# Kernel optimization log

Measured on AMD Instinct MI355X. Metric: run time of the kernel, lower is better.

Reference implementation:

```python
import jax, jax.numpy as jnp
import numpy as np

DIM = 192
HEADS = 8
B, H, W = 8, 128, 128

def _dwconv3x3(x, w):
    # x: [B,C,H,W], w: [C,1,3,3] depthwise
    return jax.lax.conv_general_dilated(
        x, w, window_strides=(1, 1), padding=((1, 1), (1, 1)),
        dimension_numbers=('NCHW', 'OIHW', 'NCHW'),
        feature_group_count=x.shape[1])

def _proj(x, pw, dw):
    # 1x1 pointwise (as einsum) followed by 3x3 depthwise
    y = jnp.einsum('bchw,oc->bohw', x, pw)
    return _dwconv3x3(y, dw)

def setup_inputs() -> dict:
    key = jax.random.key(0)
    ks = jax.random.split(key, 9)
    s_pw = 1.0 / np.sqrt(DIM)
    s_dw = 1.0 / 3.0
    return {
        'x_feat': jax.random.normal(ks[0], (B, DIM, H, W), jnp.float32),
        'y_feat': jax.random.normal(ks[1], (B, DIM, H, W), jnp.float32),
        'q_pw': jax.random.normal(ks[2], (DIM, DIM), jnp.float32) * s_pw,
        'q_dw': jax.random.normal(ks[3], (DIM, 1, 3, 3), jnp.float32) * s_dw,
        'k_pw': jax.random.normal(ks[4], (DIM, DIM), jnp.float32) * s_pw,
        'k_dw': jax.random.normal(ks[5], (DIM, 1, 3, 3), jnp.float32) * s_dw,
        'v_pw': jax.random.normal(ks[6], (DIM, DIM), jnp.float32) * s_pw,
        'v_dw': jax.random.normal(ks[7], (DIM, 1, 3, 3), jnp.float32) * s_dw,
        'proj_w': jax.random.normal(ks[8], (DIM, DIM), jnp.float32) * s_pw,
        'temperature': jnp.ones((HEADS, 1, 1), jnp.float32),
    }

def reference(x_feat, y_feat, q_pw, q_dw, k_pw, k_dw, v_pw, v_dw, proj_w, temperature):
    b, c, h, w = x_feat.shape
    ch = c // HEADS  # channels per head
    q = _proj(x_feat, q_pw, q_dw)
    k = _proj(y_feat, k_pw, k_dw)
    v = _proj(y_feat, v_pw, v_dw)
    # b (head c) h w -> b head c (h w)
    to_heads = lambda t: t.reshape(b, HEADS, ch, h * w)
    q, k, v = to_heads(q), to_heads(k), to_heads(v)
    # L2-normalize along token dim (torch F.normalize eps=1e-12)
    q = q / jnp.maximum(jnp.linalg.norm(q, axis=-1, keepdims=True), 1e-12)
    k = k / jnp.maximum(jnp.linalg.norm(k, axis=-1, keepdims=True), 1e-12)
    attn = jnp.einsum('bhcn,bhdn->bhcd', q, k) * temperature  # [b,heads,ch,ch]
    attn = jax.nn.softmax(attn, axis=-1)
    out = jnp.einsum('bhcd,bhdn->bhcn', attn, v)
    out = out.reshape(b, c, h, w)
    out = jnp.einsum('bchw,oc->bohw', out, proj_w)
    return out
```

## Files before the change

### kernel.cpp

```cpp
#include <hip/hip_runtime.h>
#include <hip/hip_bf16.h>

#define BATCH 8
#define CDIM 192
#define HEADS 8
#define CH 24
#define HH 128
#define WW 128
#define NPIX (HH*WW)
#define NELEM (BATCH*CDIM*NPIX)
#define NP4 (NPIX/4)

#define NSLAB 64
#define NJOBS 624

typedef __attribute__((ext_vector_type(8))) short bf16x8;
typedef __attribute__((ext_vector_type(4))) float f32x4;
typedef __attribute__((ext_vector_type(4))) unsigned int u32x4;
typedef unsigned int u32;
typedef const __attribute__((address_space(1))) u32* gas_ptr;
typedef __attribute__((address_space(3))) u32* las_ptr;

#define UNIT 100663296ull
__device__ __align__(256) unsigned char g_pool[6 * UNIT + (16u << 20)];

#define OFF_T0Q  (0 * UNIT)
#define OFF_T0K  (1 * UNIT)
#define OFF_T0V  (2 * UNIT)
#define OFF_Q    (3 * UNIT)
#define OFF_K    (4 * UNIT)
#define OFF_V    (5 * UNIT)
#define OFF_MISC (6 * UNIT)
#define OFF_PART (OFF_MISC)
#define OFF_S    (OFF_MISC + 10223616ull)
#define OFF_M    (OFF_S + 159744ull)
#define OFF_MF   (OFF_M + 1179648ull)

__device__ inline unsigned short bf_rne(float x) {
  unsigned u = __float_as_uint(x);
  unsigned r = (u + 0x7fffu + ((u >> 16) & 1u)) >> 16;
  return (unsigned short)r;
}
__device__ inline void f32_split(float x, unsigned short& h, unsigned short& l) {
  h = bf_rne(x);
  float hf = __uint_as_float(((unsigned)h) << 16);
  l = bf_rne(x - hf);
}

__global__ __launch_bounds__(64) void w_to_frag(const float* __restrict__ W,
                                                unsigned short* __restrict__ F,
                                                int nb) {
  const int b = blockIdx.x / 12, mf = blockIdx.x % 12;
  const int lane = threadIdx.x;
  const int row = mf * 16 + (lane & 15);
  const size_t lo = (size_t)nb * CDIM * CDIM;
#pragma unroll
  for (int ks = 0; ks < 6; ++ks) {
    const int k0 = ks * 32 + (lane >> 4) * 8;
    const float* src = W + ((size_t)b * CDIM + row) * CDIM + k0;
    bf16x8 hv, lv;
#pragma unroll
    for (int j = 0; j < 8; ++j) {
      unsigned short h, l;
      f32_split(src[j], h, l);
      hv[j] = (short)h;
      lv[j] = (short)l;
    }
    const size_t didx = (((size_t)(blockIdx.x) * 6 + ks) * 64 + lane) * 8;
    *(bf16x8*)(F + didx) = hv;
    *(bf16x8*)(F + lo + didx) = lv;
  }
}

__global__ __launch_bounds__(256, 2) void mfma_gemm192(
    const float* __restrict__ X,
    const unsigned short* __restrict__ WF, size_t w_lo,
    int w_bstride,
    float* __restrict__ Out) {
  const int bn = blockIdx.x;
  const int b = blockIdx.y;
  const int t = threadIdx.x;
  const int lane = t & 63, wid = t >> 6;
  const int wm = wid >> 1, wn = wid & 1;
  const int kq = lane >> 4;

  __shared__ float Xs[2][32][128];

  const size_t wbase = (size_t)b * w_bstride;
  const float* Xb = X + (size_t)b * CDIM * NPIX + bn * 128;
  const int pxl = wn * 64 + (lane & 15);

  int srow[4], scol4[4];
#pragma unroll
  for (int p = 0; p < 4; ++p) {
    const int f = (wid * 4 + p) * 64 + lane;
    srow[p] = f >> 5;
    scol4[p] = (f & 31) ^ (((srow[p] >> 3) & 1) << 2);
  }

  f32x4 acc[6][4];
#pragma unroll
  for (int mi = 0; mi < 6; ++mi)
#pragma unroll
    for (int ni = 0; ni < 4; ++ni) acc[mi][ni] = (f32x4){0.f, 0.f, 0.f, 0.f};

#pragma unroll
  for (int p = 0; p < 4; ++p) {
    const float* src = Xb + (size_t)(srow[p]) * NPIX + scol4[p] * 4;
    las_ptr dst = (las_ptr)(void*)(&Xs[0][0][0] + (wid * 4 + p) * 256);
    __builtin_amdgcn_global_load_lds((gas_ptr)(const void*)src, dst, 16, 0, 0);
  }
  __syncthreads();

  int cur = 0;
  for (int ks = 0; ks < 6; ++ks) {
    if (ks < 5) {
#pragma unroll
      for (int p = 0; p < 4; ++p) {
        const float* src =
            Xb + (size_t)((ks + 1) * 32 + srow[p]) * NPIX + scol4[p] * 4;
        las_ptr dst =
            (las_ptr)(void*)(&Xs[cur ^ 1][0][0] + (wid * 4 + p) * 256);
        __builtin_amdgcn_global_load_lds((gas_ptr)(const void*)src, dst, 16, 0, 0);
      }
    }

    bf16x8 Ah[6], Al[6];
#pragma unroll
    for (int mi = 0; mi < 6; ++mi) {
      const int mf = wm * 6 + mi;
      const size_t idx = wbase + (((size_t)(mf * 6 + ks)) * 64 + lane) * 8;
      Ah[mi] = *(const bf16x8*)(WF + idx);
      Al[mi] = *(const bf16x8*)(WF + w_lo + idx);
    }

    u32x4 Bh[4], Bl[4];
#pragma unroll
    for (int ni = 0; ni < 4; ++ni) {
      const int pxs = (pxl + ni * 16) ^ ((kq & 1) << 4);
#pragma unroll
      for (int jp = 0; jp < 4; ++jp) {
        const float x0 = Xs[cur][kq * 8 + 2 * jp][pxs];
        const float x1 = Xs[cur][kq * 8 + 2 * jp + 1][pxs];
        const unsigned u0 = __float_as_uint(x0);
        const unsigned u1 = __float_as_uint(x1);
        Bh[ni][jp] = (u1 & 0xffff0000u) | (u0 >> 16);
        const float rr0 = x0 - __uint_as_float(u0 & 0xffff0000u);
        const float rr1 = x1 - __uint_as_float(u1 & 0xffff0000u);
        Bl[ni][jp] = ((unsigned)bf_rne(rr1) << 16) | (unsigned)bf_rne(rr0);
      }
    }

#pragma unroll
    for (int mi = 0; mi < 6; ++mi)
#pragma unroll
      for (int ni = 0; ni < 4; ++ni) {
        const bf16x8 bh = __builtin_bit_cast(bf16x8, Bh[ni]);
        const bf16x8 bl = __builtin_bit_cast(bf16x8, Bl[ni]);
        acc[mi][ni] = __builtin_amdgcn_mfma_f32_16x16x32_bf16(
            Ah[mi], bh, acc[mi][ni], 0, 0, 0);
        acc[mi][ni] = __builtin_amdgcn_mfma_f32_16x16x32_bf16(
            Ah[mi], bl, acc[mi][ni], 0, 0, 0);
        acc[mi][ni] = __builtin_amdgcn_mfma_f32_16x16x32_bf16(
            Al[mi], bh, acc[mi][ni], 0, 0, 0);
      }

    __syncthreads();
    cur ^= 1;
  }

  const int ocol = bn * 128 + wn * 64 + (lane & 15);
  const int orow = wm * 96 + (lane >> 4) * 4;
#pragma unroll
  for (int mi = 0; mi < 6; ++mi)
#pragma unroll
    for (int r = 0; r < 4; ++r) {
      const int och = orow + mi * 16 + r;
      float* dst = Out + ((size_t)b * CDIM + och) * NPIX + ocol;
#pragma unroll
      for (int ni = 0; ni < 4; ++ni) dst[ni * 16] = acc[mi][ni][r];
    }
}

__global__ __launch_bounds__(256) void dwconv(const float* __restrict__ In,
                                              const float* __restrict__ Wd,
                                              float* __restrict__ Out) {
  const int idx = blockIdx.x * 256 + threadIdx.x;
  if (idx >= NELEM / 4) return;
  const int x4 = (idx & 31) * 4;
  const int y = (idx >> 5) & 127;
  const int c = (idx >> 12) % CDIM;
  const int b = idx / (32 * 128 * CDIM);

  const float* base = In + (size_t)(b * CDIM + c) * NPIX;
  float w[9];
#pragma unroll
  for (int i = 0; i < 9; ++i) w[i] = Wd[c * 9 + i];

  float acc0 = 0.f, acc1 = 0.f, acc2 = 0.f, acc3 = 0.f;
#pragma unroll
  for (int dy = 0; dy < 3; ++dy) {
    const int yy = y + dy - 1;
    if (yy < 0 || yy > 127) continue;
    const float* row = base + yy * WW;
    float vb0 = (x4 > 0) ? row[x4 - 1] : 0.f;
    const float4 m = *(const float4*)(row + x4);
    const float vb5 = (x4 + 4 < WW) ? row[x4 + 4] : 0.f;
    const float w0 = w[dy * 3 + 0], w1 = w[dy * 3 + 1], w2 = w[dy * 3 + 2];
    acc0 += w0 * vb0 + w1 * m.x + w2 * m.y;
    acc1 += w0 * m.x + w1 * m.y + w2 * m.z;
    acc2 += w0 * m.y + w1 * m.z + w2 * m.w;
    acc3 += w0 * m.z + w1 * m.w + w2 * vb5;
  }
  float4 o;
  o.x = acc0; o.y = acc1; o.z = acc2; o.w = acc3;
  *(float4*)(Out + (size_t)idx * 4) = o;
}

__global__ __launch_bounds__(256) void dots_partial(const float* __restrict__ Q,
                                                    const float* __restrict__ K,
                                                    float* __restrict__ Part) {
  const int bh = blockIdx.x;
  const int slab = blockIdx.y;
  const int b = bh >> 3, h = bh & 7;
  const int t = threadIdx.x;
  const int pg = t & 15;
  const int sb = t >> 4;
  const int sr = sb >> 2, sc = sb & 3;
  const bool diag = (sr == sc);

  const float4* qb = (const float4*)(Q + (size_t)(b * CDIM + h * CH) * NPIX);
  const float4* kb = (const float4*)(K + (size_t)(b * CDIM + h * CH) * NPIX);
  const int F_PER_SLAB = NP4 / NSLAB;
  const int NITER = F_PER_SLAB / 16;

  float acc[6][6];
#pragma unroll
  for (int j = 0; j < 6; ++j)
#pragma unroll
    for (int c = 0; c < 6; ++c) acc[j][c] = 0.f;
  float qq[6] = {0, 0, 0, 0, 0, 0};
  float kk[6] = {0, 0, 0, 0, 0, 0};

  const int f0 = slab * F_PER_SLAB + pg;
#pragma unroll 2
  for (int i = 0; i < NITER; ++i) {
    const int f = f0 + 16 * i;
    float4 qv[6], kv[6];
#pragma unroll
    for (int j = 0; j < 6; ++j) qv[j] = qb[(size_t)(sr * 6 + j) * NP4 + f];
#pragma unroll
    for (int j = 0; j < 6; ++j) kv[j] = kb[(size_t)(sc * 6 + j) * NP4 + f];
#pragma unroll
    for (int j = 0; j < 6; ++j)
#pragma unroll
      for (int c = 0; c < 6; ++c)
        acc[j][c] += qv[j].x * kv[c].x + qv[j].y * kv[c].y +
                     qv[j].z * kv[c].z + qv[j].w * kv[c].w;
    if (diag) {
#pragma unroll
      for (int j = 0; j < 6; ++j) {
        qq[j] += qv[j].x * qv[j].x + qv[j].y * qv[j].y + qv[j].z * qv[j].z +
                 qv[j].w * qv[j].w;
        kk[j] += kv[j].x * kv[j].x + kv[j].y * kv[j].y + kv[j].z * kv[j].z +
                 kv[j].w * kv[j].w;
      }
    }
  }

#pragma unroll
  for (int j = 0; j < 6; ++j)
#pragma unroll
    for (int c = 0; c < 6; ++c) {
      float v = acc[j][c];
      v += __shfl_xor(v, 1);
      v += __shfl_xor(v, 2);
      v += __shfl_xor(v, 4);
      v += __shfl_xor(v, 8);
      acc[j][c] = v;
    }
#pragma unroll
  for (int j = 0; j < 6; ++j) {
    float a = qq[j], bb = kk[j];
    a += __shfl_xor(a, 1); a += __shfl_xor(a, 2);
    a += __shfl_xor(a, 4); a += __shfl_xor(a, 8);
    bb += __shfl_xor(bb, 1); bb += __shfl_xor(bb, 2);
    bb += __shfl_xor(bb, 4); bb += __shfl_xor(bb, 8);
    qq[j] = a; kk[j] = bb;
  }

  if (pg == 0) {
    float* P = Part + ((size_t)bh * NSLAB + slab) * NJOBS;
#pragma unroll
    for (int j = 0; j < 6; ++j)
#pragma unroll
      for (int c = 0; c < 6; ++c)
        P[(sr * 6 + j) * 24 + sc * 6 + c] = acc[j][c];
    if (diag) {
#pragma unroll
      for (int j = 0; j < 6; ++j) {
        P[576 + sr * 6 + j] = qq[j];
        P[600 + sc * 6 + j] = kk[j];
      }
    }
  }
}

__global__ __launch_bounds__(640) void dots_reduce(const float* __restrict__ Part,
                                                   float* __restrict__ S) {
  const int bh = blockIdx.x;
  const int job = threadIdx.x;
  if (job >= NJOBS) return;
  float s = 0.f;
  for (int i = 0; i < NSLAB; ++i)
    s += Part[((size_t)bh * NSLAB + i) * NJOBS + job];
  S[bh * NJOBS + job] = s;
}

__global__ __launch_bounds__(576) void build_M(const float* __restrict__ S,
                                               const float* __restrict__ PW,
                                               const float* __restrict__ Temp,
                                               float* __restrict__ M) {
  const int b = blockIdx.x, h = blockIdx.y;
  const int bh = b * 8 + h;
  __shared__ float att[CH][CH];
  __shared__ float qn[CH], kn[CH];
  const int t = threadIdx.x;
  const float* Sb = S + (size_t)bh * NJOBS;

  if (t < CH) {
    qn[t] = fmaxf(sqrtf(Sb[576 + t]), 1e-12f);
    kn[t] = fmaxf(sqrtf(Sb[600 + t]), 1e-12f);
  }
  __syncthreads();
  const float temp = Temp[h];
  if (t < 576) {
    const int c = t / 24, d = t % 24;
    att[c][d] = Sb[t] / (qn[c] * kn[d]) * temp;
  }
  __syncthreads();
  if (t < CH) {
    float mx = -1e30f;
    for (int d = 0; d < CH; ++d) mx = fmaxf(mx, att[t][d]);
    float sum = 0.f;
    for (int d = 0; d < CH; ++d) {
      const float e = __expf(att[t][d] - mx);
      att[t][d] = e;
      sum += e;
    }
    const float inv = 1.f / sum;
    for (int d = 0; d < CH; ++d) att[t][d] *= inv;
  }
  __syncthreads();
  for (int i = t; i < CDIM * CH; i += 576) {
    const int o = i / CH, d = i % CH;
    float s = 0.f;
#pragma unroll
    for (int c = 0; c < CH; ++c) s += PW[o * CDIM + h * CH + c] * att[c][d];
    M[((size_t)b * CDIM + o) * CDIM + h * CH + d] = s;
  }
}


extern "C" void kernel_launch(void* const* d_in, const int* in_sizes, int n_in,
                              void* d_out, int out_size, void* d_ws, size_t ws_size,
                              hipStream_t stream) {
  const float* x_feat = (const float*)d_in[0];
  const float* y_feat = (const float*)d_in[1];
  const float* q_pw   = (const float*)d_in[2];
  const float* q_dw   = (const float*)d_in[3];
  const float* k_pw   = (const float*)d_in[4];
  const float* k_dw   = (const float*)d_in[5];
  const float* v_pw   = (const float*)d_in[6];
  const float* v_dw   = (const float*)d_in[7];
  const float* proj_w = (const float*)d_in[8];
  const float* temp   = (const float*)d_in[9];
  float* out = (float*)d_out;

  unsigned char* pool;
  (void)hipGetSymbolAddress((void**)&pool, HIP_SYMBOL(g_pool));
  float* t0q = (float*)(pool + OFF_T0Q);
  float* t0k = (float*)(pool + OFF_T0K);
  float* t0v = (float*)(pool + OFF_T0V);
  float* q  = (float*)(pool + OFF_Q);
  float* k  = (float*)(pool + OFF_K);
  float* v  = (float*)(pool + OFF_V);
  float* part = (float*)(pool + OFF_PART);
  float* S    = (float*)(pool + OFF_S);
  float* M    = (float*)(pool + OFF_M);
  unsigned short* MF = (unsigned short*)(pool + OFF_MF);

  unsigned short* WQF = MF + 2ull * 8 * CDIM * CDIM;
  unsigned short* WKF = WQF + 2ull * CDIM * CDIM;
  unsigned short* WVF = WKF + 2ull * CDIM * CDIM;

  const size_t w1_lo = (size_t)1 * CDIM * CDIM;
  const size_t w8_lo = (size_t)8 * CDIM * CDIM;

  const dim3 ggrid(NPIX / 128, BATCH);
  const int dwgrid = (NELEM / 4) / 256;

  w_to_frag<<<12, 64, 0, stream>>>(q_pw, WQF, 1);
  w_to_frag<<<12, 64, 0, stream>>>(k_pw, WKF, 1);
  w_to_frag<<<12, 64, 0, stream>>>(v_pw, WVF, 1);

  mfma_gemm192<<<ggrid, 256, 0, stream>>>(x_feat, WQF, w1_lo, 0, t0q);
  dwconv<<<dwgrid, 256, 0, stream>>>(t0q, q_dw, q);
  mfma_gemm192<<<ggrid, 256, 0, stream>>>(y_feat, WKF, w1_lo, 0, t0k);
  dwconv<<<dwgrid, 256, 0, stream>>>(t0k, k_dw, k);

  dots_partial<<<dim3(64, NSLAB), 256, 0, stream>>>(q, k, part);
  dots_reduce<<<64, 640, 0, stream>>>(part, S);
  build_M<<<dim3(BATCH, HEADS), 576, 0, stream>>>(S, proj_w, temp, M);
  w_to_frag<<<8 * 12, 64, 0, stream>>>(M, MF, 8);

  mfma_gemm192<<<ggrid, 256, 0, stream>>>(y_feat, WVF, w1_lo, 0, t0v);
  dwconv<<<dwgrid, 256, 0, stream>>>(t0v, v_dw, v);

  mfma_gemm192<<<ggrid, 256, 0, stream>>>(v, MF, w8_lo, CDIM * CDIM, out);
}
```

Before: 470.9 us.

## Compute Q·K Gram and norms with split-bf16 MFMA from bf16 dwconv outputs

The q and k depthwise convolutions now write hi/lo bf16 split pairs instead of fp32. A new MFMA kernel computes the per-head 24x24 Q·K^T Gram matrix and the squared row norms using three-term split-bf16 products, replacing the scalar FP32 dot kernel. The slab count drops from 64 to 16, and one shared temporary buffer replaces three. The q/k tensors keep the same byte size, but the dot computation moves onto matrix cores. The cost is extra MFMA work spent on wasted tile padding (24 rows padded to 32) and a small loss of precision from dropping the lo*lo term.

```diff
diff --git a/kernel.cpp b/kernel.cpp
--- a/kernel.cpp
+++ b/kernel.cpp
@@ -11,28 +11,27 @@
 #define NELEM (BATCH*CDIM*NPIX)
 #define NP4 (NPIX/4)
 
-#define NSLAB 64
+#define DSLAB 16
 #define NJOBS 624
 
 typedef __attribute__((ext_vector_type(8))) short bf16x8;
 typedef __attribute__((ext_vector_type(4))) float f32x4;
 typedef __attribute__((ext_vector_type(4))) unsigned int u32x4;
+typedef __attribute__((ext_vector_type(4))) unsigned short u16x4;
 typedef unsigned int u32;
 typedef const __attribute__((address_space(1))) u32* gas_ptr;
 typedef __attribute__((address_space(3))) u32* las_ptr;
 
 #define UNIT 100663296ull
-__device__ __align__(256) unsigned char g_pool[6 * UNIT + (16u << 20)];
-
-#define OFF_T0Q  (0 * UNIT)
-#define OFF_T0K  (1 * UNIT)
-#define OFF_T0V  (2 * UNIT)
-#define OFF_Q    (3 * UNIT)
-#define OFF_K    (4 * UNIT)
-#define OFF_V    (5 * UNIT)
-#define OFF_MISC (6 * UNIT)
+__device__ __align__(256) unsigned char g_pool[4 * UNIT + (16u << 20)];
+
+#define OFF_T0   (0 * UNIT)
+#define OFF_QB   (1 * UNIT)
+#define OFF_KB   (2 * UNIT)
+#define OFF_V    (3 * UNIT)
+#define OFF_MISC (4 * UNIT)
 #define OFF_PART (OFF_MISC)
-#define OFF_S    (OFF_MISC + 10223616ull)
+#define OFF_S    (OFF_MISC + 2555904ull)
 #define OFF_M    (OFF_S + 159744ull)
 #define OFF_MF   (OFF_M + 1179648ull)
 
@@ -217,92 +216,143 @@
   *(float4*)(Out + (size_t)idx * 4) = o;
 }
 
-__global__ __launch_bounds__(256) void dots_partial(const float* __restrict__ Q,
-                                                    const float* __restrict__ K,
-                                                    float* __restrict__ Part) {
+__global__ __launch_bounds__(256) void dwconv_bf(const float* __restrict__ In,
+                                                 const float* __restrict__ Wd,
+                                                 unsigned short* __restrict__ Out) {
+  const int idx = blockIdx.x * 256 + threadIdx.x;
+  if (idx >= NELEM / 4) return;
+  const int x4 = (idx & 31) * 4;
+  const int y = (idx >> 5) & 127;
+  const int c = (idx >> 12) % CDIM;
+  const int b = idx / (32 * 128 * CDIM);
+
+  const float* base = In + (size_t)(b * CDIM + c) * NPIX;
+  float w[9];
+#pragma unroll
+  for (int i = 0; i < 9; ++i) w[i] = Wd[c * 9 + i];
+
+  float a[4] = {0.f, 0.f, 0.f, 0.f};
+#pragma unroll
+  for (int dy = 0; dy < 3; ++dy) {
+    const int yy = y + dy - 1;
+    if (yy < 0 || yy > 127) continue;
+    const float* row = base + yy * WW;
+    float vb0 = (x4 > 0) ? row[x4 - 1] : 0.f;
+    const float4 m = *(const float4*)(row + x4);
+    const float vb5 = (x4 + 4 < WW) ? row[x4 + 4] : 0.f;
+    const float w0 = w[dy * 3 + 0], w1 = w[dy * 3 + 1], w2 = w[dy * 3 + 2];
+    a[0] += w0 * vb0 + w1 * m.x + w2 * m.y;
+    a[1] += w0 * m.x + w1 * m.y + w2 * m.z;
+    a[2] += w0 * m.y + w1 * m.z + w2 * m.w;
+    a[3] += w0 * m.z + w1 * m.w + w2 * vb5;
+  }
+  u16x4 hv, lv;
+#pragma unroll
+  for (int j = 0; j < 4; ++j) {
+    unsigned short h, l;
+    f32_split(a[j], h, l);
+    hv[j] = h;
+    lv[j] = l;
+  }
+  *(u16x4*)(Out + (size_t)idx * 4) = hv;
+  *(u16x4*)(Out + NELEM + (size_t)idx * 4) = lv;
+}
+
+__global__ __launch_bounds__(256) void dots_mfma(
+    const unsigned short* __restrict__ QF,
+    const unsigned short* __restrict__ KF,
+    float* __restrict__ Part) {
   const int bh = blockIdx.x;
   const int slab = blockIdx.y;
   const int b = bh >> 3, h = bh & 7;
   const int t = threadIdx.x;
-  const int pg = t & 15;
-  const int sb = t >> 4;
-  const int sr = sb >> 2, sc = sb & 3;
-  const bool diag = (sr == sc);
-
-  const float4* qb = (const float4*)(Q + (size_t)(b * CDIM + h * CH) * NPIX);
-  const float4* kb = (const float4*)(K + (size_t)(b * CDIM + h * CH) * NPIX);
-  const int F_PER_SLAB = NP4 / NSLAB;
-  const int NITER = F_PER_SLAB / 16;
-
-  float acc[6][6];
-#pragma unroll
-  for (int j = 0; j < 6; ++j)
-#pragma unroll
-    for (int c = 0; c < 6; ++c) acc[j][c] = 0.f;
-  float qq[6] = {0, 0, 0, 0, 0, 0};
-  float kk[6] = {0, 0, 0, 0, 0, 0};
-
-  const int f0 = slab * F_PER_SLAB + pg;
-#pragma unroll 2
-  for (int i = 0; i < NITER; ++i) {
-    const int f = f0 + 16 * i;
-    float4 qv[6], kv[6];
-#pragma unroll
-    for (int j = 0; j < 6; ++j) qv[j] = qb[(size_t)(sr * 6 + j) * NP4 + f];
-#pragma unroll
-    for (int j = 0; j < 6; ++j) kv[j] = kb[(size_t)(sc * 6 + j) * NP4 + f];
-#pragma unroll
-    for (int j = 0; j < 6; ++j)
-#pragma unroll
-      for (int c = 0; c < 6; ++c)
-        acc[j][c] += qv[j].x * kv[c].x + qv[j].y * kv[c].y +
-                     qv[j].z * kv[c].z + qv[j].w * kv[c].w;
-    if (diag) {
-#pragma unroll
-      for (int j = 0; j < 6; ++j) {
-        qq[j] += qv[j].x * qv[j].x + qv[j].y * qv[j].y + qv[j].z * qv[j].z +
-                 qv[j].w * qv[j].w;
-        kk[j] += kv[j].x * kv[j].x + kv[j].y * kv[j].y + kv[j].z * kv[j].z +
-                 kv[j].w * kv[j].w;
+  const int lane = t & 63, wid = t >> 6;
+
+  const size_t rowbase = (size_t)(b * CDIM + h * CH);
+  const int px0 = slab * 1024 + wid * 256;
+  const int rr = lane & 15;
+  const int j8 = (lane >> 4) * 8;
+
+  f32x4 accx[2][2], aqq[2], aqhl[2], akk[2], akhl[2];
+#pragma unroll
+  for (int mi = 0; mi < 2; ++mi) {
+#pragma unroll
+    for (int ni = 0; ni < 2; ++ni) accx[mi][ni] = (f32x4){0.f, 0.f, 0.f, 0.f};
+    aqq[mi] = (f32x4){0.f, 0.f, 0.f, 0.f};
+    aqhl[mi] = (f32x4){0.f, 0.f, 0.f, 0.f};
+    akk[mi] = (f32x4){0.f, 0.f, 0.f, 0.f};
+    akhl[mi] = (f32x4){0.f, 0.f, 0.f, 0.f};
+  }
+
+#pragma unroll
+  for (int s = 0; s < 8; ++s) {
+    const int px = px0 + s * 32 + j8;
+    bf16x8 qh[2], ql[2], kh[2], kl[2];
+#pragma unroll
+    for (int mi = 0; mi < 2; ++mi) {
+      const size_t off = (rowbase + mi * 16 + rr) * (size_t)NPIX + px;
+      qh[mi] = *(const bf16x8*)(QF + off);
+      ql[mi] = *(const bf16x8*)(QF + NELEM + off);
+      kh[mi] = *(const bf16x8*)(KF + off);
+      kl[mi] = *(const bf16x8*)(KF + NELEM + off);
+    }
+#pragma unroll
+    for (int mi = 0; mi < 2; ++mi) {
+#pragma unroll
+      for (int ni = 0; ni < 2; ++ni) {
+        accx[mi][ni] = __builtin_amdgcn_mfma_f32_16x16x32_bf16(
+            qh[mi], kh[ni], accx[mi][ni], 0, 0, 0);
+        accx[mi][ni] = __builtin_amdgcn_mfma_f32_16x16x32_bf16(
+            qh[mi], kl[ni], accx[mi][ni], 0, 0, 0);
+        accx[mi][ni] = __builtin_amdgcn_mfma_f32_16x16x32_bf16(
+            ql[mi], kh[ni], accx[mi][ni], 0, 0, 0);
       }
-    }
-  }
-
-#pragma unroll
-  for (int j = 0; j < 6; ++j)
-#pragma unroll
-    for (int c = 0; c < 6; ++c) {
-      float v = acc[j][c];
-      v += __shfl_xor(v, 1);
-      v += __shfl_xor(v, 2);
-      v += __shfl_xor(v, 4);
-      v += __shfl_xor(v, 8);
-      acc[j][c] = v;
-    }
-#pragma unroll
-  for (int j = 0; j < 6; ++j) {
-    float a = qq[j], bb = kk[j];
-    a += __shfl_xor(a, 1); a += __shfl_xor(a, 2);
-    a += __shfl_xor(a, 4); a += __shfl_xor(a, 8);
-    bb += __shfl_xor(bb, 1); bb += __shfl_xor(bb, 2);
-    bb += __shfl_xor(bb, 4); bb += __shfl_xor(bb, 8);
-    qq[j] = a; kk[j] = bb;
-  }
-
-  if (pg == 0) {
-    float* P = Part + ((size_t)bh * NSLAB + slab) * NJOBS;
-#pragma unroll
-    for (int j = 0; j < 6; ++j)
-#pragma unroll
-      for (int c = 0; c < 6; ++c)
-        P[(sr * 6 + j) * 24 + sc * 6 + c] = acc[j][c];
-    if (diag) {
-#pragma unroll
-      for (int j = 0; j < 6; ++j) {
-        P[576 + sr * 6 + j] = qq[j];
-        P[600 + sc * 6 + j] = kk[j];
+      aqq[mi] = __builtin_amdgcn_mfma_f32_16x16x32_bf16(qh[mi], qh[mi],
+                                                        aqq[mi], 0, 0, 0);
+      aqhl[mi] = __builtin_amdgcn_mfma_f32_16x16x32_bf16(qh[mi], ql[mi],
+                                                         aqhl[mi], 0, 0, 0);
+      akk[mi] = __builtin_amdgcn_mfma_f32_16x16x32_bf16(kh[mi], kh[mi],
+                                                        akk[mi], 0, 0, 0);
+      akhl[mi] = __builtin_amdgcn_mfma_f32_16x16x32_bf16(kh[mi], kl[mi],
+                                                         akhl[mi], 0, 0, 0);
+    }
+  }
+
+  __shared__ float xls[4][24][24];
+  __shared__ float qls[4][24], kls[4][24];
+  const int col = lane & 15;
+  const int rbase = (lane >> 4) * 4;
+#pragma unroll
+  for (int mi = 0; mi < 2; ++mi) {
+#pragma unroll
+    for (int ni = 0; ni < 2; ++ni) {
+      const int d = ni * 16 + col;
+      if (d < 24) {
+#pragma unroll
+        for (int r = 0; r < 4; ++r) {
+          const int c = mi * 16 + rbase + r;
+          if (c < 24) xls[wid][c][d] = accx[mi][ni][r];
+        }
       }
     }
+    const int cc = mi * 16 + col;
+    const int rd = col - rbase;
+    if (cc < 24 && rd >= 0 && rd < 4) {
+      qls[wid][cc] = aqq[mi][rd] + 2.f * aqhl[mi][rd];
+      kls[wid][cc] = akk[mi][rd] + 2.f * akhl[mi][rd];
+    }
+  }
+  __syncthreads();
+
+  float* P = Part + ((size_t)bh * DSLAB + slab) * NJOBS;
+  for (int j = t; j < 576; j += 256) {
+    const int c = j / 24, d = j % 24;
+    P[j] = xls[0][c][d] + xls[1][c][d] + xls[2][c][d] + xls[3][c][d];
+  }
+  if (t < 24) P[576 + t] = qls[0][t] + qls[1][t] + qls[2][t] + qls[3][t];
+  else if (t >= 32 && t < 56) {
+    const int c = t - 32;
+    P[600 + c] = kls[0][c] + kls[1][c] + kls[2][c] + kls[3][c];
   }
 }
 
@@ -312,8 +362,8 @@
   const int job = threadIdx.x;
   if (job >= NJOBS) return;
   float s = 0.f;
-  for (int i = 0; i < NSLAB; ++i)
-    s += Part[((size_t)bh * NSLAB + i) * NJOBS + job];
+  for (int i = 0; i < DSLAB; ++i)
+    s += Part[((size_t)bh * DSLAB + i) * NJOBS + job];
   S[bh * NJOBS + job] = s;
 }
 
@@ -379,11 +429,9 @@
 
   unsigned char* pool;
   (void)hipGetSymbolAddress((void**)&pool, HIP_SYMBOL(g_pool));
-  float* t0q = (float*)(pool + OFF_T0Q);
-  float* t0k = (float*)(pool + OFF_T0K);
-  float* t0v = (float*)(pool + OFF_T0V);
-  float* q  = (float*)(pool + OFF_Q);
-  float* k  = (float*)(pool + OFF_K);
+  float* t0 = (float*)(pool + OFF_T0);
+  unsigned short* QB = (unsigned short*)(pool + OFF_QB);
+  unsigned short* KB = (unsigned short*)(pool + OFF_KB);
   float* v  = (float*)(pool + OFF_V);
   float* part = (float*)(pool + OFF_PART);
   float* S    = (float*)(pool + OFF_S);
@@ -404,18 +452,18 @@
   w_to_frag<<<12, 64, 0, stream>>>(k_pw, WKF, 1);
   w_to_frag<<<12, 64, 0, stream>>>(v_pw, WVF, 1);
 
-  mfma_gemm192<<<ggrid, 256, 0, stream>>>(x_feat, WQF, w1_lo, 0, t0q);
-  dwconv<<<dwgrid, 256, 0, stream>>>(t0q, q_dw, q);
-  mfma_gemm192<<<ggrid, 256, 0, stream>>>(y_feat, WKF, w1_lo, 0, t0k);
-  dwconv<<<dwgrid, 256, 0, stream>>>(t0k, k_dw, k);
-
-  dots_partial<<<dim3(64, NSLAB), 256, 0, stream>>>(q, k, part);
+  mfma_gemm192<<<ggrid, 256, 0, stream>>>(x_feat, WQF, w1_lo, 0, t0);
+  dwconv_bf<<<dwgrid, 256, 0, stream>>>(t0, q_dw, QB);
+  mfma_gemm192<<<ggrid, 256, 0, stream>>>(y_feat, WKF, w1_lo, 0, t0);
+  dwconv_bf<<<dwgrid, 256, 0, stream>>>(t0, k_dw, KB);
+
+  dots_mfma<<<dim3(64, DSLAB), 256, 0, stream>>>(QB, KB, part);
   dots_reduce<<<64, 640, 0, stream>>>(part, S);
   build_M<<<dim3(BATCH, HEADS), 576, 0, stream>>>(S, proj_w, temp, M);
   w_to_frag<<<8 * 12, 64, 0, stream>>>(M, MF, 8);
 
-  mfma_gemm192<<<ggrid, 256, 0, stream>>>(y_feat, WVF, w1_lo, 0, t0v);
-  dwconv<<<dwgrid, 256, 0, stream>>>(t0v, v_dw, v);
+  mfma_gemm192<<<ggrid, 256, 0, stream>>>(y_feat, WVF, w1_lo, 0, t0);
+  dwconv<<<dwgrid, 256, 0, stream>>>(t0, v_dw, v);
 
   mfma_gemm192<<<ggrid, 256, 0, stream>>>(v, MF, w8_lo, CDIM * CDIM, out);
 }
```

Result: faster. 455.1 us (-3.3%).
